# Kernel optimization log

Measured on AMD Instinct MI355X. Metric: run time of the kernel, lower is better.

## Reference

```python
import jax, jax.numpy as jnp
import numpy as np

C = 256
DF = 8
CQK = C // DF  # 32


def setup_inputs() -> dict:
    key = jax.random.key(0)
    ks = jax.random.split(key, 7)
    s = 0.02
    x = jax.random.normal(ks[0], (4, C, 64, 64), dtype=jnp.float32)
    Wq = jax.random.normal(ks[1], (CQK, C), dtype=jnp.float32) * s
    bq = jnp.zeros((CQK,), dtype=jnp.float32)
    Wk = jax.random.normal(ks[2], (CQK, C), dtype=jnp.float32) * s
    bk = jnp.zeros((CQK,), dtype=jnp.float32)
    Wv = jax.random.normal(ks[3], (C, C), dtype=jnp.float32) * s
    bv = jnp.zeros((C,), dtype=jnp.float32)
    gamma = jnp.ones((1,), dtype=jnp.float32)  # nonzero so output is nontrivial
    return {"x": x, "Wq": Wq, "bq": bq, "Wk": Wk, "bk": bk, "Wv": Wv, "bv": bv, "gamma": gamma}


def reference(x, Wq, bq, Wk, bk, Wv, bv, gamma):
    B, Cc, H, W = x.shape
    # flatten spatial: [B, N, C] with N = H*W
    xf = x.reshape(B, Cc, H * W).transpose(0, 2, 1)
    # 1x1 convs == per-pixel linear projections
    q = jnp.einsum('bnc,dc->bnd', xf, Wq) + bq        # [B, N, Cqk]
    k = jnp.einsum('bnc,dc->bnd', xf, Wk) + bk        # [B, N, Cqk]
    v = jnp.einsum('bnc,dc->bnd', xf, Wv) + bv        # [B, N, C]
    energy = jnp.einsum('bnd,bmd->bnm', q, k)          # [B, N, N], no scale (as in source)
    attn = jax.nn.softmax(energy, axis=-1)
    out = jnp.einsum('bnm,bmc->bnc', attn, v)          # [B, N, C]
    out = out.transpose(0, 2, 1).reshape(B, Cc, H, W)
    return gamma[0] * out
```

## Files before the change

kernel.cpp:

```cpp
#include <hip/hip_runtime.h>
#include <hip/hip_bf16.h>


typedef __attribute__((ext_vector_type(8))) short s8v;
typedef __attribute__((ext_vector_type(4))) float f4v;

#define NPIX 4096
#define CIN 256
#define DQK 32

#if __has_builtin(__builtin_amdgcn_exp2f)
#define EXP2(x) __builtin_amdgcn_exp2f(x)
#else
#define EXP2(x) exp2f(x)
#endif

static __device__ __forceinline__ unsigned short f2bf(float f) {
    union { float f; unsigned int u; } v; v.f = f;
    unsigned int r = v.u + 0x7FFF + ((v.u >> 16) & 1);
    return (unsigned short)(r >> 16);
}
static __device__ __forceinline__ unsigned int fbits(float f) {
    union { float f; unsigned int u; } v; v.f = f; return v.u;
}

__global__ void wcast_kernel(const float* __restrict__ Wq, const float* __restrict__ bq,
                             const float* __restrict__ Wk, const float* __restrict__ bk,
                             const float* __restrict__ Wv, const float* __restrict__ bv,
                             unsigned short* __restrict__ Wall, float* __restrict__ ball) {
    int row = blockIdx.x;
    int t = threadIdx.x;
    const float* src; const float* bsrc;
    if (row < 32)       { src = Wq + row * 256;        bsrc = bq + row; }
    else if (row < 64)  { src = Wk + (row - 32) * 256; bsrc = bk + (row - 32); }
    else                { src = Wv + (row - 64) * 256; bsrc = bv + (row - 64); }
    Wall[row * 256 + t] = f2bf(src[t]);
    if (t == 0) ball[row] = bsrc[0];
}

__global__ void tcast_kernel(const float* __restrict__ x, unsigned short* __restrict__ xT) {
    __shared__ unsigned short tile[64][65];
    int bidx = blockIdx.x;
    int b    = bidx >> 8;
    int cblk = (bidx >> 6) & 3;
    int nblk = bidx & 63;
    int t = threadIdx.x;
    int c0 = cblk * 64, n0 = nblk * 64;
    const float* xb = x + (size_t)b * CIN * NPIX;
    #pragma unroll
    for (int p = 0; p < 4; p++) {
        int cl = p * 16 + (t >> 4);
        int nl = (t & 15) * 4;
        float4 v = *(const float4*)(xb + (size_t)(c0 + cl) * NPIX + n0 + nl);
        tile[cl][nl + 0] = f2bf(v.x);
        tile[cl][nl + 1] = f2bf(v.y);
        tile[cl][nl + 2] = f2bf(v.z);
        tile[cl][nl + 3] = f2bf(v.w);
    }
    __syncthreads();
    unsigned short* xTb = xT + (size_t)b * NPIX * CIN;
    #pragma unroll
    for (int p = 0; p < 4; p++) {
        int nl = p * 16 + (t >> 4);
        int cl = (t & 15) * 4;
        ushort4 wv;
        wv.x = tile[cl + 0][nl];
        wv.y = tile[cl + 1][nl];
        wv.z = tile[cl + 2][nl];
        wv.w = tile[cl + 3][nl];
        *(ushort4*)(xTb + (size_t)(n0 + nl) * CIN + c0 + cl) = wv;
    }
}

__global__ __launch_bounds__(256)
void proj_kernel(const unsigned short* __restrict__ xT,
                 const unsigned short* __restrict__ Wall,
                 const float* __restrict__ ball,
                 unsigned short* __restrict__ Q,
                 unsigned short* __restrict__ Kp,
                 unsigned short* __restrict__ Vt) {
    int idx  = blockIdx.x;
    int b    = (idx & 7) >> 1;
    int nblk = ((idx >> 3) << 1) | (idx & 1);
    int w    = threadIdx.x >> 6;
    int lane = threadIdx.x & 63;
    int l16 = lane & 15, quad = lane >> 4;
    int n0 = nblk * 64 + w * 16;

    const unsigned short* brow = xT + (size_t)(b * NPIX + n0 + l16) * CIN + quad * 8;
    s8v bfr[8];
    #pragma unroll
    for (int kk = 0; kk < 8; kk++) bfr[kk] = *(const s8v*)(brow + kk * 32);

    #pragma unroll
    for (int p = 0; p < 10; p++) {
        const unsigned short* w0 = Wall + (size_t)(2 * p * 16 + l16) * CIN + quad * 8;
        const unsigned short* w1 = w0 + 16 * CIN;
        f4v a0 = {0.f, 0.f, 0.f, 0.f}, a1 = {0.f, 0.f, 0.f, 0.f};
        if (p < 2) {
            #pragma unroll
            for (int kk = 0; kk < 8; kk++) {
                a0 = __builtin_amdgcn_mfma_f32_16x16x32_bf16(bfr[kk], *(const s8v*)(w0 + kk * 32), a0, 0, 0, 0);
                a1 = __builtin_amdgcn_mfma_f32_16x16x32_bf16(bfr[kk], *(const s8v*)(w1 + kk * 32), a1, 0, 0, 0);
            }
        } else {
            #pragma unroll
            for (int kk = 0; kk < 8; kk++) {
                a0 = __builtin_amdgcn_mfma_f32_16x16x32_bf16(*(const s8v*)(w0 + kk * 32), bfr[kk], a0, 0, 0, 0);
                a1 = __builtin_amdgcn_mfma_f32_16x16x32_bf16(*(const s8v*)(w1 + kk * 32), bfr[kk], a1, 0, 0, 0);
            }
        }
        #pragma unroll
        for (int half = 0; half < 2; half++) {
            int ob = 2 * p + half;
            f4v acc = half ? a1 : a0;
            if (ob < 2) {
                int oc = ob * 16 + l16;
                float bias = ball[oc];
                #pragma unroll
                for (int r = 0; r < 4; r++) {
                    int n = n0 + quad * 4 + r;
                    Q[(size_t)(b * NPIX + n) * DQK + oc] =
                        f2bf((acc[r] + bias) * 1.44269504f);
                }
            } else if (ob < 4) {
                int oc = (ob - 2) * 16 + l16;
                float bias = ball[32 + oc];
                #pragma unroll
                for (int r = 0; r < 4; r++) {
                    int n = n0 + quad * 4 + r;
                    int pn = (n & ~31) | (((n >> 2) & 1) << 4) | (((n >> 3) & 3) << 2) | (n & 3);
                    Kp[(size_t)(b * NPIX + pn) * DQK + oc] = f2bf(acc[r] + bias);
                }
            } else {
                int n = n0 + l16;
                #pragma unroll
                for (int r = 0; r < 4; r++) {
                    int ch = (ob - 4) * 16 + quad * 4 + r;
                    Vt[((size_t)b * CIN + ch) * NPIX + n] = f2bf(acc[r] + ball[64 + ch]);
                }
            }
        }
    }
}

#define ATTN_STEP(KC0, KC1, VC, KN0, KN1, VN, NKV)                              \
    {                                                                           \
        KN0 = *(const s8v*)(kbase + (NKV) * DQK);                               \
        KN1 = *(const s8v*)(kbase + ((NKV) + 16) * DQK);                        \
        _Pragma("unroll")                                                       \
        for (int ct = 0; ct < 4; ct++)                                          \
            VN[ct] = *(const s8v*)(vbase + ct * 16 * NPIX + (NKV));             \
        s8v pu[4];                                                              \
        _Pragma("unroll")                                                       \
        for (int rt = 0; rt < 4; rt++) {                                        \
            f4v s0 = {0.f, 0.f, 0.f, 0.f}, s1 = {0.f, 0.f, 0.f, 0.f};           \
            s0 = __builtin_amdgcn_mfma_f32_16x16x32_bf16(KC0, qf[rt], s0, 0, 0, 0); \
            s1 = __builtin_amdgcn_mfma_f32_16x16x32_bf16(KC1, qf[rt], s1, 0, 0, 0); \
            float p00 = EXP2(s0[0]), p01 = EXP2(s0[1]);                         \
            float p02 = EXP2(s0[2]), p03 = EXP2(s0[3]);                         \
            float p10 = EXP2(s1[0]), p11 = EXP2(s1[1]);                         \
            float p12 = EXP2(s1[2]), p13 = EXP2(s1[3]);                         \
            lsum[rt] += ((p00 + p01) + (p02 + p03)) + ((p10 + p11) + (p12 + p13)); \
            union { uint4 u; s8v v; } pp;                                       \
            pp.u.x = __builtin_amdgcn_perm(fbits(p01), fbits(p00), 0x07060302); \
            pp.u.y = __builtin_amdgcn_perm(fbits(p03), fbits(p02), 0x07060302); \
            pp.u.z = __builtin_amdgcn_perm(fbits(p11), fbits(p10), 0x07060302); \
            pp.u.w = __builtin_amdgcn_perm(fbits(p13), fbits(p12), 0x07060302); \
            pu[rt] = pp.v;                                                      \
        }                                                                       \
        _Pragma("unroll")                                                       \
        for (int ct = 0; ct < 4; ct++)                                          \
            _Pragma("unroll")                                                   \
            for (int rt = 0; rt < 4; rt++)                                      \
                O[rt][ct] = __builtin_amdgcn_mfma_f32_16x16x32_bf16(VC[ct], pu[rt], O[rt][ct], 0, 0, 0); \
    }

__global__ __launch_bounds__(512, 2)
void attn_kernel(const unsigned short* __restrict__ Q,
                 const unsigned short* __restrict__ Kp,
                 const unsigned short* __restrict__ Vt,
                 const float* __restrict__ gamma,
                 float* __restrict__ out) {
    __shared__ float ldsO[4][64][68];
    __shared__ float ldsL[4][16];

    int idx = blockIdx.x;
    int b      = (idx & 7) >> 1;
    int rowblk = ((idx >> 3) << 1) | (idx & 1);

    int lane = threadIdx.x & 63;
    int w    = threadIdx.x >> 6;
    int l16 = lane & 15, quad = lane >> 4;
    int kh = w >> 2;
    int cs = w & 3;

    const unsigned short* Kb = Kp + (size_t)b * NPIX * DQK;
    const unsigned short* Vb = Vt + (size_t)b * CIN * NPIX;

    int rowbase = rowblk * 64;
    s8v qf[4];
    #pragma unroll
    for (int rt = 0; rt < 4; rt++)
        qf[rt] = *(const s8v*)(Q + (size_t)(b * NPIX + rowbase + rt * 16 + l16) * DQK + quad * 8);

    const unsigned short* kbase = Kb + (32 * kh + l16) * DQK + quad * 8;
    const unsigned short* vbase = Vb + (size_t)(cs * 64 + l16) * NPIX + 32 * kh + quad * 8;

    f4v O[4][4];
    #pragma unroll
    for (int rt = 0; rt < 4; rt++)
        #pragma unroll
        for (int ct = 0; ct < 4; ct++) O[rt][ct] = (f4v){0.f, 0.f, 0.f, 0.f};
    float lsum[4] = {0.f, 0.f, 0.f, 0.f};

    s8v Vc[4], Vn[4], Kc0, Kc1, Kn0, Kn1;
    Kc0 = *(const s8v*)(kbase);
    Kc1 = *(const s8v*)(kbase + 16 * DQK);
    #pragma unroll
    for (int ct = 0; ct < 4; ct++)
        Vc[ct] = *(const s8v*)(vbase + ct * 16 * NPIX);

    for (int kv2 = 0; kv2 < NPIX; kv2 += 128) {
        ATTN_STEP(Kc0, Kc1, Vc, Kn0, Kn1, Vn, kv2 + 64);
        ATTN_STEP(Kn0, Kn1, Vn, Kc0, Kc1, Vc, (kv2 + 128) & (NPIX - 1));
    }

    #pragma unroll
    for (int rt = 0; rt < 4; rt++) {
        lsum[rt] += __shfl_xor(lsum[rt], 16);
        lsum[rt] += __shfl_xor(lsum[rt], 32);
    }

    if (kh == 1) {
        #pragma unroll
        for (int rt = 0; rt < 4; rt++)
            #pragma unroll
            for (int ct = 0; ct < 4; ct++)
                *(f4v*)&ldsO[cs][lane][(rt * 4 + ct) * 4] = O[rt][ct];
        if (cs == 0 && quad == 0) {
            #pragma unroll
            for (int rt = 0; rt < 4; rt++) ldsL[rt][l16] = lsum[rt];
        }
    }
    __syncthreads();

    if (kh == 0) {
        float g = gamma[0];
        float rinv[4];
        #pragma unroll
        for (int rt = 0; rt < 4; rt++)
            rinv[rt] = g / (lsum[rt] + ldsL[rt][l16]);
        #pragma unroll
        for (int rt = 0; rt < 4; rt++) {
            #pragma unroll
            for (int ct = 0; ct < 4; ct++) {
                f4v o2 = *(const f4v*)&ldsO[cs][lane][(rt * 4 + ct) * 4];
                #pragma unroll
                for (int r = 0; r < 4; r++) {
                    int ch = cs * 64 + ct * 16 + quad * 4 + r;
                    out[((size_t)b * CIN + ch) * NPIX + rowbase + rt * 16 + l16] =
                        (O[rt][ct][r] + o2[r]) * rinv[rt];
                }
            }
        }
    }
}

extern "C" void kernel_launch(void* const* d_in, const int* in_sizes, int n_in,
                              void* d_out, int out_size, void* d_ws, size_t ws_size,
                              hipStream_t stream) {
    const float* x     = (const float*)d_in[0];
    const float* Wq    = (const float*)d_in[1];
    const float* bq    = (const float*)d_in[2];
    const float* Wk    = (const float*)d_in[3];
    const float* bk    = (const float*)d_in[4];
    const float* Wv    = (const float*)d_in[5];
    const float* bv    = (const float*)d_in[6];
    const float* gamma = (const float*)d_in[7];
    float* out = (float*)d_out;

    char* p = (char*)d_ws;
    unsigned short* xT   = (unsigned short*)p; p += (size_t)4 * NPIX * CIN * 2;
    unsigned short* Qb   = (unsigned short*)p; p += (size_t)4 * NPIX * DQK * 2;
    unsigned short* Kb   = (unsigned short*)p; p += (size_t)4 * NPIX * DQK * 2;
    unsigned short* Vt   = (unsigned short*)p; p += (size_t)4 * CIN * NPIX * 2;
    unsigned short* Wall = (unsigned short*)p; p += (size_t)320 * 256 * 2;
    float*          ball = (float*)p;          p += (size_t)320 * 4;

    wcast_kernel<<<320, 256, 0, stream>>>(Wq, bq, Wk, bk, Wv, bv, Wall, ball);
    tcast_kernel<<<1024, 256, 0, stream>>>(x, xT);
    proj_kernel<<<256, 256, 0, stream>>>(xT, Wall, ball, Qb, Kb, Vt);
    attn_kernel<<<256, 512, 0, stream>>>(Qb, Kb, Vt, gamma, out);
}
```

Before: 185.1 us.

## Split attention KV loop four ways per block and spread projection over more blocks

```diff
diff --git a/kernel.cpp b/kernel.cpp
--- a/kernel.cpp
+++ b/kernel.cpp
@@ -79,7 +79,9 @@
                  unsigned short* __restrict__ Q,
                  unsigned short* __restrict__ Kp,
                  unsigned short* __restrict__ Vt) {
-    int idx  = blockIdx.x;
+    int g    = blockIdx.x;
+    int oq   = g >> 8;
+    int idx  = g & 255;
     int b    = (idx & 7) >> 1;
     int nblk = ((idx >> 3) << 1) | (idx & 1);
     int w    = threadIdx.x >> 6;
@@ -93,11 +95,12 @@
     for (int kk = 0; kk < 8; kk++) bfr[kk] = *(const s8v*)(brow + kk * 32);
 
     #pragma unroll
-    for (int p = 0; p < 10; p++) {
-        const unsigned short* w0 = Wall + (size_t)(2 * p * 16 + l16) * CIN + quad * 8;
+    for (int pp = 0; pp < 2; pp++) {
+        int ob0 = oq * 4 + 2 * pp;
+        const unsigned short* w0 = Wall + (size_t)(ob0 * 16 + l16) * CIN + quad * 8;
         const unsigned short* w1 = w0 + 16 * CIN;
         f4v a0 = {0.f, 0.f, 0.f, 0.f}, a1 = {0.f, 0.f, 0.f, 0.f};
-        if (p < 2) {
+        if (ob0 < 4) {
             #pragma unroll
             for (int kk = 0; kk < 8; kk++) {
                 a0 = __builtin_amdgcn_mfma_f32_16x16x32_bf16(bfr[kk], *(const s8v*)(w0 + kk * 32), a0, 0, 0, 0);
@@ -112,7 +115,7 @@
         }
         #pragma unroll
         for (int half = 0; half < 2; half++) {
-            int ob = 2 * p + half;
+            int ob = ob0 + half;
             f4v acc = half ? a1 : a0;
             if (ob < 2) {
                 int oc = ob * 16 + l16;
@@ -176,14 +179,14 @@
                 O[rt][ct] = __builtin_amdgcn_mfma_f32_16x16x32_bf16(VC[ct], pu[rt], O[rt][ct], 0, 0, 0); \
     }
 
-__global__ __launch_bounds__(512, 2)
+__global__ __launch_bounds__(1024, 4)
 void attn_kernel(const unsigned short* __restrict__ Q,
                  const unsigned short* __restrict__ Kp,
                  const unsigned short* __restrict__ Vt,
                  const float* __restrict__ gamma,
                  float* __restrict__ out) {
     __shared__ float ldsO[4][64][68];
-    __shared__ float ldsL[4][16];
+    __shared__ float ldsL[3][4][16];
 
     int idx = blockIdx.x;
     int b      = (idx & 7) >> 1;
@@ -221,9 +224,9 @@
     for (int ct = 0; ct < 4; ct++)
         Vc[ct] = *(const s8v*)(vbase + ct * 16 * NPIX);
 
-    for (int kv2 = 0; kv2 < NPIX; kv2 += 128) {
-        ATTN_STEP(Kc0, Kc1, Vc, Kn0, Kn1, Vn, kv2 + 64);
-        ATTN_STEP(Kn0, Kn1, Vn, Kc0, Kc1, Vc, (kv2 + 128) & (NPIX - 1));
+    for (int kv2 = 0; kv2 < NPIX; kv2 += 256) {
+        ATTN_STEP(Kc0, Kc1, Vc, Kn0, Kn1, Vn, kv2 + 128);
+        ATTN_STEP(Kn0, Kn1, Vn, Kc0, Kc1, Vc, (kv2 + 256) & (NPIX - 1));
     }
 
     #pragma unroll
@@ -231,36 +234,45 @@
         lsum[rt] += __shfl_xor(lsum[rt], 16);
         lsum[rt] += __shfl_xor(lsum[rt], 32);
     }
-
-    if (kh == 1) {
-        #pragma unroll
-        for (int rt = 0; rt < 4; rt++)
-            #pragma unroll
-            for (int ct = 0; ct < 4; ct++)
-                *(f4v*)&ldsO[cs][lane][(rt * 4 + ct) * 4] = O[rt][ct];
-        if (cs == 0 && quad == 0) {
-            #pragma unroll
-            for (int rt = 0; rt < 4; rt++) ldsL[rt][l16] = lsum[rt];
-        }
-    }
-    __syncthreads();
+    if (kh > 0 && cs == 0 && quad == 0) {
+        #pragma unroll
+        for (int rt = 0; rt < 4; rt++) ldsL[kh - 1][rt][l16] = lsum[rt];
+    }
+
+    for (int j = 1; j <= 3; j++) {
+        if (kh == j) {
+            #pragma unroll
+            for (int rt = 0; rt < 4; rt++)
+                #pragma unroll
+                for (int ct = 0; ct < 4; ct++)
+                    *(f4v*)&ldsO[cs][lane][(rt * 4 + ct) * 4] = O[rt][ct];
+        }
+        __syncthreads();
+        if (kh == 0) {
+            #pragma unroll
+            for (int rt = 0; rt < 4; rt++)
+                #pragma unroll
+                for (int ct = 0; ct < 4; ct++)
+                    O[rt][ct] += *(const f4v*)&ldsO[cs][lane][(rt * 4 + ct) * 4];
+        }
+        __syncthreads();
+    }
 
     if (kh == 0) {
         float g = gamma[0];
         float rinv[4];
         #pragma unroll
         for (int rt = 0; rt < 4; rt++)
-            rinv[rt] = g / (lsum[rt] + ldsL[rt][l16]);
+            rinv[rt] = g / (lsum[rt] + ldsL[0][rt][l16] + ldsL[1][rt][l16] + ldsL[2][rt][l16]);
         #pragma unroll
         for (int rt = 0; rt < 4; rt++) {
             #pragma unroll
             for (int ct = 0; ct < 4; ct++) {
-                f4v o2 = *(const f4v*)&ldsO[cs][lane][(rt * 4 + ct) * 4];
                 #pragma unroll
                 for (int r = 0; r < 4; r++) {
                     int ch = cs * 64 + ct * 16 + quad * 4 + r;
                     out[((size_t)b * CIN + ch) * NPIX + rowbase + rt * 16 + l16] =
-                        (O[rt][ct][r] + o2[r]) * rinv[rt];
+                        O[rt][ct][r] * rinv[rt];
                 }
             }
         }
@@ -290,6 +302,6 @@
 
     wcast_kernel<<<320, 256, 0, stream>>>(Wq, bq, Wk, bk, Wv, bv, Wall, ball);
     tcast_kernel<<<1024, 256, 0, stream>>>(x, xT);
-    proj_kernel<<<256, 256, 0, stream>>>(xT, Wall, ball, Qb, Kb, Vt);
-    attn_kernel<<<256, 512, 0, stream>>>(Qb, Kb, Vt, gamma, out);
-}
+    proj_kernel<<<1280, 256, 0, stream>>>(xT, Wall, ball, Qb, Kb, Vt);
+    attn_kernel<<<256, 1024, 0, stream>>>(Qb, Kb, Vt, gamma, out);
+}
```

New measurement: 472.5 us. 155% more time.

## Fuse weight cast, transpose and projection; halve attention row tile for occupancy

Applied to the files above, without the earlier changes.

```diff
diff --git a/kernel.cpp b/kernel.cpp
--- a/kernel.cpp
+++ b/kernel.cpp
@@ -23,137 +23,133 @@
 static __device__ __forceinline__ unsigned int fbits(float f) {
     union { float f; unsigned int u; } v; v.f = f; return v.u;
 }
-
-__global__ void wcast_kernel(const float* __restrict__ Wq, const float* __restrict__ bq,
-                             const float* __restrict__ Wk, const float* __restrict__ bk,
-                             const float* __restrict__ Wv, const float* __restrict__ bv,
-                             unsigned short* __restrict__ Wall, float* __restrict__ ball) {
-    int row = blockIdx.x;
-    int t = threadIdx.x;
-    const float* src; const float* bsrc;
-    if (row < 32)       { src = Wq + row * 256;        bsrc = bq + row; }
-    else if (row < 64)  { src = Wk + (row - 32) * 256; bsrc = bk + (row - 32); }
-    else                { src = Wv + (row - 64) * 256; bsrc = bv + (row - 64); }
-    Wall[row * 256 + t] = f2bf(src[t]);
-    if (t == 0) ball[row] = bsrc[0];
-}
-
-__global__ void tcast_kernel(const float* __restrict__ x, unsigned short* __restrict__ xT) {
-    __shared__ unsigned short tile[64][65];
-    int bidx = blockIdx.x;
-    int b    = bidx >> 8;
-    int cblk = (bidx >> 6) & 3;
-    int nblk = bidx & 63;
-    int t = threadIdx.x;
-    int c0 = cblk * 64, n0 = nblk * 64;
-    const float* xb = x + (size_t)b * CIN * NPIX;
-    #pragma unroll
-    for (int p = 0; p < 4; p++) {
-        int cl = p * 16 + (t >> 4);
-        int nl = (t & 15) * 4;
-        float4 v = *(const float4*)(xb + (size_t)(c0 + cl) * NPIX + n0 + nl);
-        tile[cl][nl + 0] = f2bf(v.x);
-        tile[cl][nl + 1] = f2bf(v.y);
-        tile[cl][nl + 2] = f2bf(v.z);
-        tile[cl][nl + 3] = f2bf(v.w);
-    }
-    __syncthreads();
-    unsigned short* xTb = xT + (size_t)b * NPIX * CIN;
-    #pragma unroll
-    for (int p = 0; p < 4; p++) {
-        int nl = p * 16 + (t >> 4);
-        int cl = (t & 15) * 4;
-        ushort4 wv;
-        wv.x = tile[cl + 0][nl];
-        wv.y = tile[cl + 1][nl];
-        wv.z = tile[cl + 2][nl];
-        wv.w = tile[cl + 3][nl];
-        *(ushort4*)(xTb + (size_t)(n0 + nl) * CIN + c0 + cl) = wv;
-    }
+static __device__ __forceinline__ s8v loadpack_bf16(const float* p) {
+    float4 a = *(const float4*)p;
+    float4 b = *(const float4*)(p + 4);
+    union { unsigned short us[8]; s8v v; } u;
+    u.us[0] = f2bf(a.x); u.us[1] = f2bf(a.y); u.us[2] = f2bf(a.z); u.us[3] = f2bf(a.w);
+    u.us[4] = f2bf(b.x); u.us[5] = f2bf(b.y); u.us[6] = f2bf(b.z); u.us[7] = f2bf(b.w);
+    return u.v;
 }
 
 __global__ __launch_bounds__(256)
-void proj_kernel(const unsigned short* __restrict__ xT,
-                 const unsigned short* __restrict__ Wall,
-                 const float* __restrict__ ball,
+void prep_kernel(const float* __restrict__ x,
+                 const float* __restrict__ Wq, const float* __restrict__ bq,
+                 const float* __restrict__ Wk, const float* __restrict__ bk,
+                 const float* __restrict__ Wv, const float* __restrict__ bv,
                  unsigned short* __restrict__ Q,
                  unsigned short* __restrict__ Kp,
                  unsigned short* __restrict__ Vt) {
-    int idx  = blockIdx.x;
-    int b    = (idx & 7) >> 1;
-    int nblk = ((idx >> 3) << 1) | (idx & 1);
-    int w    = threadIdx.x >> 6;
-    int lane = threadIdx.x & 63;
+    __shared__ unsigned short xLDS[32 * 256];
+
+    int idx = blockIdx.x;
+    int b   = (idx & 7) >> 1;
+    int nb  = ((idx >> 3) << 1) | (idx & 1);
+    int n0  = nb * 32;
+    int t   = threadIdx.x;
+
+    {
+        int nloc  = (t & 7) * 4;
+        int cbase = t >> 3;
+        const float* xb = x + (size_t)b * CIN * NPIX + n0 + nloc;
+        #pragma unroll
+        for (int i = 0; i < 8; i++) {
+            int c = i * 32 + cbase;
+            float4 v = *(const float4*)(xb + (size_t)c * NPIX);
+            int kk = c >> 5, quad = (c >> 3) & 3, off = c & 7;
+            unsigned short* dst = &xLDS[((kk * 4 + quad) * 32) * 8 + off];
+            dst[(nloc + 0) * 8] = f2bf(v.x);
+            dst[(nloc + 1) * 8] = f2bf(v.y);
+            dst[(nloc + 2) * 8] = f2bf(v.z);
+            dst[(nloc + 3) * 8] = f2bf(v.w);
+        }
+    }
+    __syncthreads();
+
+    int lane = t & 63, w = t >> 6;
     int l16 = lane & 15, quad = lane >> 4;
-    int n0 = nblk * 64 + w * 16;
-
-    const unsigned short* brow = xT + (size_t)(b * NPIX + n0 + l16) * CIN + quad * 8;
+    int wr = w & 1, wo = w >> 1;
+    int nrow0 = 16 * wr;
+
     s8v bfr[8];
     #pragma unroll
-    for (int kk = 0; kk < 8; kk++) bfr[kk] = *(const s8v*)(brow + kk * 32);
-
-    #pragma unroll
-    for (int p = 0; p < 10; p++) {
-        const unsigned short* w0 = Wall + (size_t)(2 * p * 16 + l16) * CIN + quad * 8;
-        const unsigned short* w1 = w0 + 16 * CIN;
-        f4v a0 = {0.f, 0.f, 0.f, 0.f}, a1 = {0.f, 0.f, 0.f, 0.f};
-        if (p < 2) {
+    for (int kk = 0; kk < 8; kk++)
+        bfr[kk] = *(const s8v*)&xLDS[(((kk * 4 + quad) * 32) + nrow0 + l16) * 8];
+
+    #pragma unroll
+    for (int pp = 0; pp < 5; pp++) {
+        int ob0 = wo * 10 + 2 * pp;
+        const float* wsrc; const float* bsrc; int rowbase_w;
+        if (ob0 < 2)      { wsrc = Wq; bsrc = bq; rowbase_w = ob0 * 16; }
+        else if (ob0 < 4) { wsrc = Wk; bsrc = bk; rowbase_w = (ob0 - 2) * 16; }
+        else              { wsrc = Wv; bsrc = bv; rowbase_w = (ob0 - 4) * 16; }
+        const float* w0p = wsrc + (size_t)(rowbase_w + l16) * CIN + quad * 8;
+        const float* w1p = w0p + 16 * CIN;
+
+        f4v acc0 = {0.f, 0.f, 0.f, 0.f}, acc1 = {0.f, 0.f, 0.f, 0.f};
+        if (ob0 < 4) {
             #pragma unroll
             for (int kk = 0; kk < 8; kk++) {
-                a0 = __builtin_amdgcn_mfma_f32_16x16x32_bf16(bfr[kk], *(const s8v*)(w0 + kk * 32), a0, 0, 0, 0);
-                a1 = __builtin_amdgcn_mfma_f32_16x16x32_bf16(bfr[kk], *(const s8v*)(w1 + kk * 32), a1, 0, 0, 0);
+                s8v w0f = loadpack_bf16(w0p + kk * 32);
+                s8v w1f = loadpack_bf16(w1p + kk * 32);
+                acc0 = __builtin_amdgcn_mfma_f32_16x16x32_bf16(bfr[kk], w0f, acc0, 0, 0, 0);
+                acc1 = __builtin_amdgcn_mfma_f32_16x16x32_bf16(bfr[kk], w1f, acc1, 0, 0, 0);
             }
         } else {
             #pragma unroll
             for (int kk = 0; kk < 8; kk++) {
-                a0 = __builtin_amdgcn_mfma_f32_16x16x32_bf16(*(const s8v*)(w0 + kk * 32), bfr[kk], a0, 0, 0, 0);
-                a1 = __builtin_amdgcn_mfma_f32_16x16x32_bf16(*(const s8v*)(w1 + kk * 32), bfr[kk], a1, 0, 0, 0);
-            }
-        }
+                s8v w0f = loadpack_bf16(w0p + kk * 32);
+                s8v w1f = loadpack_bf16(w1p + kk * 32);
+                acc0 = __builtin_amdgcn_mfma_f32_16x16x32_bf16(w0f, bfr[kk], acc0, 0, 0, 0);
+                acc1 = __builtin_amdgcn_mfma_f32_16x16x32_bf16(w1f, bfr[kk], acc1, 0, 0, 0);
+            }
+        }
+
         #pragma unroll
         for (int half = 0; half < 2; half++) {
-            int ob = 2 * p + half;
-            f4v acc = half ? a1 : a0;
+            int ob = ob0 + half;
+            f4v acc = half ? acc1 : acc0;
             if (ob < 2) {
                 int oc = ob * 16 + l16;
-                float bias = ball[oc];
-                #pragma unroll
-                for (int r = 0; r < 4; r++) {
-                    int n = n0 + quad * 4 + r;
+                float bias = bsrc[oc];
+                #pragma unroll
+                for (int r = 0; r < 4; r++) {
+                    int n = n0 + nrow0 + quad * 4 + r;
                     Q[(size_t)(b * NPIX + n) * DQK + oc] =
                         f2bf((acc[r] + bias) * 1.44269504f);
                 }
             } else if (ob < 4) {
                 int oc = (ob - 2) * 16 + l16;
-                float bias = ball[32 + oc];
-                #pragma unroll
-                for (int r = 0; r < 4; r++) {
-                    int n = n0 + quad * 4 + r;
+                float bias = bsrc[oc];
+                #pragma unroll
+                for (int r = 0; r < 4; r++) {
+                    int n = n0 + nrow0 + quad * 4 + r;
                     int pn = (n & ~31) | (((n >> 2) & 1) << 4) | (((n >> 3) & 3) << 2) | (n & 3);
                     Kp[(size_t)(b * NPIX + pn) * DQK + oc] = f2bf(acc[r] + bias);
                 }
             } else {
-                int n = n0 + l16;
+                int n = n0 + nrow0 + l16;
                 #pragma unroll
                 for (int r = 0; r < 4; r++) {
                     int ch = (ob - 4) * 16 + quad * 4 + r;
-                    Vt[((size_t)b * CIN + ch) * NPIX + n] = f2bf(acc[r] + ball[64 + ch]);
-                }
-            }
-        }
-    }
-}
-
-#define ATTN_STEP(KC0, KC1, VC, KN0, KN1, VN, NKV)                              \
+                    Vt[((size_t)b * CIN + ch) * NPIX + n] = f2bf(acc[r] + bsrc[ch]);
+                }
+            }
+        }
+    }
+}
+
+#define ATTN_STEP(KC0, KC1, KN0, KN1, NKV_NEXT, NKV_CUR)                        \
     {                                                                           \
-        KN0 = *(const s8v*)(kbase + (NKV) * DQK);                               \
-        KN1 = *(const s8v*)(kbase + ((NKV) + 16) * DQK);                        \
+        KN0 = *(const s8v*)(kbase + (NKV_NEXT) * DQK);                          \
+        KN1 = *(const s8v*)(kbase + ((NKV_NEXT) + 16) * DQK);                   \
+        s8v Vc[4];                                                              \
         _Pragma("unroll")                                                       \
         for (int ct = 0; ct < 4; ct++)                                          \
-            VN[ct] = *(const s8v*)(vbase + ct * 16 * NPIX + (NKV));             \
-        s8v pu[4];                                                              \
+            Vc[ct] = *(const s8v*)(vbase + ct * 16 * NPIX + (NKV_CUR));         \
+        s8v pu[2];                                                              \
         _Pragma("unroll")                                                       \
-        for (int rt = 0; rt < 4; rt++) {                                        \
+        for (int rt = 0; rt < 2; rt++) {                                        \
             f4v s0 = {0.f, 0.f, 0.f, 0.f}, s1 = {0.f, 0.f, 0.f, 0.f};           \
             s0 = __builtin_amdgcn_mfma_f32_16x16x32_bf16(KC0, qf[rt], s0, 0, 0, 0); \
             s1 = __builtin_amdgcn_mfma_f32_16x16x32_bf16(KC1, qf[rt], s1, 0, 0, 0); \
@@ -172,18 +168,18 @@
         _Pragma("unroll")                                                       \
         for (int ct = 0; ct < 4; ct++)                                          \
             _Pragma("unroll")                                                   \
-            for (int rt = 0; rt < 4; rt++)                                      \
-                O[rt][ct] = __builtin_amdgcn_mfma_f32_16x16x32_bf16(VC[ct], pu[rt], O[rt][ct], 0, 0, 0); \
-    }
-
-__global__ __launch_bounds__(512, 2)
+            for (int rt = 0; rt < 2; rt++)                                      \
+                O[rt][ct] = __builtin_amdgcn_mfma_f32_16x16x32_bf16(Vc[ct], pu[rt], O[rt][ct], 0, 0, 0); \
+    }
+
+__global__ __launch_bounds__(512, 4)
 void attn_kernel(const unsigned short* __restrict__ Q,
                  const unsigned short* __restrict__ Kp,
                  const unsigned short* __restrict__ Vt,
                  const float* __restrict__ gamma,
                  float* __restrict__ out) {
-    __shared__ float ldsO[4][64][68];
-    __shared__ float ldsL[4][16];
+    __shared__ float ldsO[4][64][34];
+    __shared__ float ldsL[2][16];
 
     int idx = blockIdx.x;
     int b      = (idx & 7) >> 1;
@@ -198,61 +194,58 @@
     const unsigned short* Kb = Kp + (size_t)b * NPIX * DQK;
     const unsigned short* Vb = Vt + (size_t)b * CIN * NPIX;
 
-    int rowbase = rowblk * 64;
-    s8v qf[4];
-    #pragma unroll
-    for (int rt = 0; rt < 4; rt++)
+    int rowbase = rowblk * 32;
+    s8v qf[2];
+    #pragma unroll
+    for (int rt = 0; rt < 2; rt++)
         qf[rt] = *(const s8v*)(Q + (size_t)(b * NPIX + rowbase + rt * 16 + l16) * DQK + quad * 8);
 
     const unsigned short* kbase = Kb + (32 * kh + l16) * DQK + quad * 8;
     const unsigned short* vbase = Vb + (size_t)(cs * 64 + l16) * NPIX + 32 * kh + quad * 8;
 
-    f4v O[4][4];
-    #pragma unroll
-    for (int rt = 0; rt < 4; rt++)
+    f4v O[2][4];
+    #pragma unroll
+    for (int rt = 0; rt < 2; rt++)
         #pragma unroll
         for (int ct = 0; ct < 4; ct++) O[rt][ct] = (f4v){0.f, 0.f, 0.f, 0.f};
-    float lsum[4] = {0.f, 0.f, 0.f, 0.f};
-
-    s8v Vc[4], Vn[4], Kc0, Kc1, Kn0, Kn1;
+    float lsum[2] = {0.f, 0.f};
+
+    s8v Kc0, Kc1, Kn0, Kn1;
     Kc0 = *(const s8v*)(kbase);
     Kc1 = *(const s8v*)(kbase + 16 * DQK);
-    #pragma unroll
-    for (int ct = 0; ct < 4; ct++)
-        Vc[ct] = *(const s8v*)(vbase + ct * 16 * NPIX);
 
     for (int kv2 = 0; kv2 < NPIX; kv2 += 128) {
-        ATTN_STEP(Kc0, Kc1, Vc, Kn0, Kn1, Vn, kv2 + 64);
-        ATTN_STEP(Kn0, Kn1, Vn, Kc0, Kc1, Vc, (kv2 + 128) & (NPIX - 1));
-    }
-
-    #pragma unroll
-    for (int rt = 0; rt < 4; rt++) {
+        ATTN_STEP(Kc0, Kc1, Kn0, Kn1, kv2 + 64, kv2);
+        ATTN_STEP(Kn0, Kn1, Kc0, Kc1, (kv2 + 128) & (NPIX - 1), kv2 + 64);
+    }
+
+    #pragma unroll
+    for (int rt = 0; rt < 2; rt++) {
         lsum[rt] += __shfl_xor(lsum[rt], 16);
         lsum[rt] += __shfl_xor(lsum[rt], 32);
     }
 
     if (kh == 1) {
         #pragma unroll
-        for (int rt = 0; rt < 4; rt++)
+        for (int rt = 0; rt < 2; rt++)
             #pragma unroll
             for (int ct = 0; ct < 4; ct++)
                 *(f4v*)&ldsO[cs][lane][(rt * 4 + ct) * 4] = O[rt][ct];
         if (cs == 0 && quad == 0) {
             #pragma unroll
-            for (int rt = 0; rt < 4; rt++) ldsL[rt][l16] = lsum[rt];
+            for (int rt = 0; rt < 2; rt++) ldsL[rt][l16] = lsum[rt];
         }
     }
     __syncthreads();
 
     if (kh == 0) {
         float g = gamma[0];
-        float rinv[4];
-        #pragma unroll
-        for (int rt = 0; rt < 4; rt++)
+        float rinv[2];
+        #pragma unroll
+        for (int rt = 0; rt < 2; rt++)
             rinv[rt] = g / (lsum[rt] + ldsL[rt][l16]);
         #pragma unroll
-        for (int rt = 0; rt < 4; rt++) {
+        for (int rt = 0; rt < 2; rt++) {
             #pragma unroll
             for (int ct = 0; ct < 4; ct++) {
                 f4v o2 = *(const f4v*)&ldsO[cs][lane][(rt * 4 + ct) * 4];
@@ -281,15 +274,10 @@
     float* out = (float*)d_out;
 
     char* p = (char*)d_ws;
-    unsigned short* xT   = (unsigned short*)p; p += (size_t)4 * NPIX * CIN * 2;
-    unsigned short* Qb   = (unsigned short*)p; p += (size_t)4 * NPIX * DQK * 2;
-    unsigned short* Kb   = (unsigned short*)p; p += (size_t)4 * NPIX * DQK * 2;
-    unsigned short* Vt   = (unsigned short*)p; p += (size_t)4 * CIN * NPIX * 2;
-    unsigned short* Wall = (unsigned short*)p; p += (size_t)320 * 256 * 2;
-    float*          ball = (float*)p;          p += (size_t)320 * 4;
-
-    wcast_kernel<<<320, 256, 0, stream>>>(Wq, bq, Wk, bk, Wv, bv, Wall, ball);
-    tcast_kernel<<<1024, 256, 0, stream>>>(x, xT);
-    proj_kernel<<<256, 256, 0, stream>>>(xT, Wall, ball, Qb, Kb, Vt);
-    attn_kernel<<<256, 512, 0, stream>>>(Qb, Kb, Vt, gamma, out);
-}
+    unsigned short* Qb = (unsigned short*)p; p += (size_t)4 * NPIX * DQK * 2;
+    unsigned short* Kb = (unsigned short*)p; p += (size_t)4 * NPIX * DQK * 2;
+    unsigned short* Vt = (unsigned short*)p; p += (size_t)4 * CIN * NPIX * 2;
+
+    prep_kernel<<<512, 256, 0, stream>>>(x, Wq, bq, Wk, bk, Wv, bv, Qb, Kb, Vt);
+    attn_kernel<<<512, 512, 0, stream>>>(Qb, Kb, Vt, gamma, out);
+}
```

After: 266.9 us. 44.2% more time.
